# Optimization experiments

Measured on AMD Instinct MI355X. Metric: run time of the kernel, lower is better.

## Reference

```python
import jax, jax.numpy as jnp
import numpy as np

N_NODES = 50000
N_EDGES = 1000000
NODE_IN = 64
EDGE_OUT = 64
NODE_OUT = 64
GLOBAL_DIM = 64
N_GRAPHS = 64


def _glorot(key, shape):
    fan_in = shape[0]
    return (jax.random.normal(key, shape, dtype=jnp.float32) / jnp.sqrt(jnp.float32(fan_in)))


def setup_inputs() -> dict:
    key = jax.random.key(0)
    ks = jax.random.split(key, 12)
    x = jax.random.normal(ks[0], (N_NODES, NODE_IN), dtype=jnp.float32)
    edge_index = jax.random.randint(ks[1], (2, N_EDGES), 0, N_NODES, dtype=jnp.int64 if jax.config.jax_enable_x64 else jnp.int32)
    edge_attr = jax.random.normal(ks[2], (N_EDGES, EDGE_OUT), dtype=jnp.float32)
    u = jax.random.normal(ks[3], (N_GRAPHS, GLOBAL_DIM), dtype=jnp.float32)
    batch = jnp.sort(jax.random.randint(ks[4], (N_NODES,), 0, N_GRAPHS, dtype=jnp.int64 if jax.config.jax_enable_x64 else jnp.int32))
    # node_mlp_1: Linear(node_in+edge_out -> node_out), ReLU, Linear(node_out -> node_out)
    W1 = _glorot(ks[5], (NODE_IN + EDGE_OUT, NODE_OUT))
    b1 = jnp.zeros((NODE_OUT,), dtype=jnp.float32)
    W2 = _glorot(ks[6], (NODE_OUT, NODE_OUT))
    b2 = jnp.zeros((NODE_OUT,), dtype=jnp.float32)
    # node_mlp_2: Linear(global_dim+node_in+node_out -> node_out), ReLU, Linear(node_out -> node_out)
    W3 = _glorot(ks[7], (GLOBAL_DIM + NODE_IN + NODE_OUT, NODE_OUT))
    b3 = jnp.zeros((NODE_OUT,), dtype=jnp.float32)
    W4 = _glorot(ks[8], (NODE_OUT, NODE_OUT))
    b4 = jnp.zeros((NODE_OUT,), dtype=jnp.float32)
    return {"x": x, "edge_index": edge_index, "edge_attr": edge_attr, "u": u, "batch": batch,
            "W1": W1, "b1": b1, "W2": W2, "b2": b2, "W3": W3, "b3": b3, "W4": W4, "b4": b4}


def reference(x, edge_index, edge_attr, u, batch, W1, b1, W2, b2, W3, b3, W4, b4):
    row, col = edge_index[0], edge_index[1]
    # per-edge MLP on [x[row] || edge_attr]  -> [E, node_out]
    e = jnp.concatenate([x[row], edge_attr], axis=1)
    e = jnp.maximum(e @ W1 + b1, 0.0) @ W2 + b2
    # scatter_mean over destination nodes (zero where a node has no incoming edges)
    sums = jax.ops.segment_sum(e, col, num_segments=N_NODES)
    counts = jax.ops.segment_sum(jnp.ones((e.shape[0],), dtype=e.dtype), col, num_segments=N_NODES)
    agg = sums / jnp.clip(counts, 1.0)[:, None]
    # per-node MLP on [x || agg || u[batch]]
    h = jnp.concatenate([x, agg, u[batch]], axis=1)
    return jnp.maximum(h @ W3 + b3, 0.0) @ W4 + b4
```

## Files before the change

### kernel.cpp

```cpp
#include <hip/hip_runtime.h>

#define E_TOTAL 1000000
#define NN 50000
#define NB_SCAN ((NN + 255) / 256)

typedef __attribute__((ext_vector_type(8))) short bf16x8;
typedef __attribute__((ext_vector_type(8))) __bf16 bfv8;
typedef __attribute__((ext_vector_type(4))) float f32x4;
typedef __attribute__((ext_vector_type(4))) unsigned short u16x4;
typedef __attribute__((ext_vector_type(8))) unsigned short u16x8;

__device__ __forceinline__ float bf2f(unsigned short u) {
  unsigned int x = ((unsigned int)u) << 16;
  return __builtin_bit_cast(float, x);
}

__device__ __forceinline__ unsigned short f2bf(float v) {
  __bf16 b = (__bf16)v;
  return __builtin_bit_cast(unsigned short, b);
}

__device__ __forceinline__ bf16x8 pack8(float4 u, float4 v) {
  bfv8 f;
  f[0] = (__bf16)u.x; f[1] = (__bf16)u.y; f[2] = (__bf16)u.z; f[3] = (__bf16)u.w;
  f[4] = (__bf16)v.x; f[5] = (__bf16)v.y; f[6] = (__bf16)v.z; f[7] = (__bf16)v.w;
  return __builtin_bit_cast(bf16x8, f);
}

__device__ __forceinline__ bf16x8 cvt8(const float* __restrict__ p) {
  return pack8(*reinterpret_cast<const float4*>(p), *reinterpret_cast<const float4*>(p + 4));
}

__global__ void conv_kernel(const float* __restrict__ x, unsigned short* __restrict__ xb) {
  const int i = blockIdx.x * 256 + threadIdx.x;
  if (i < NN * 8) {
    const float4 v0 = *reinterpret_cast<const float4*>(x + (size_t)i * 8);
    const float4 v1 = *reinterpret_cast<const float4*>(x + (size_t)i * 8 + 4);
    bf16x8 p = pack8(v0, v1);
    *reinterpret_cast<bf16x8*>(xb + (size_t)i * 8) = p;
  }
}

__global__ void w3p_kernel(const float* __restrict__ W2, const float* __restrict__ W3,
                           const float* __restrict__ b2, float* __restrict__ W3p,
                           float* __restrict__ bb) {
  const int idx = blockIdx.x * 256 + threadIdx.x;
  if (idx < 64 * 64) {
    const int i = idx >> 6, j = idx & 63;
    float s = 0.f;
#pragma unroll 8
    for (int k = 0; k < 64; ++k) s += W2[i * 64 + k] * W3[(64 + k) * 64 + j];
    W3p[(64 + i) * 64 + j] = s;
    W3p[i * 64 + j] = W3[i * 64 + j];
    W3p[(128 + i) * 64 + j] = W3[(128 + i) * 64 + j];
  } else if (idx < 64 * 64 + 64) {
    const int j = idx - 64 * 64;
    float s = 0.f;
#pragma unroll 8
    for (int k = 0; k < 64; ++k) s += b2[k] * W3[(64 + k) * 64 + j];
    bb[j] = s;
  }
}


__global__ void hist_kernel(const int* __restrict__ ei, int* __restrict__ cnt) {
  int i = blockIdx.x * blockDim.x + threadIdx.x;
  if (i < E_TOTAL) atomicAdd(cnt + ei[E_TOTAL + i], 1);
}

__global__ void scan_block_kernel(const int* __restrict__ cnt, int* __restrict__ offs,
                                  int* __restrict__ btot) {
  __shared__ int s[256];
  const int tid = threadIdx.x;
  const int i = blockIdx.x * 256 + tid;
  int v = (i < NN) ? cnt[i] : 0;
  s[tid] = v;
  __syncthreads();
#pragma unroll
  for (int d = 1; d < 256; d <<= 1) {
    int t = (tid >= d) ? s[tid - d] : 0;
    __syncthreads();
    s[tid] += t;
    __syncthreads();
  }
  int incl = s[tid];
  if (i < NN) offs[i] = incl - v;
  if (tid == 255) btot[blockIdx.x] = incl;
}

__global__ void scan_add_kernel(int* __restrict__ offs, const int* __restrict__ btot,
                                int* __restrict__ run) {
  __shared__ int s[256];
  const int tid = threadIdx.x, bid = blockIdx.x;
  s[tid] = (tid < bid && tid < NB_SCAN) ? btot[tid] : 0;
  __syncthreads();
#pragma unroll
  for (int d = 128; d > 0; d >>= 1) {
    if (tid < d) s[tid] += s[tid + d];
    __syncthreads();
  }
  const int base = s[0];
  const int i = bid * 256 + tid;
  if (i < NN) {
    int o = offs[i] + base;
    offs[i] = o;
    run[i] = o;
  }
  if (i == 0) offs[NN] = E_TOTAL;
}

__global__ __launch_bounds__(512) void edge_kernel(
    const unsigned short* __restrict__ xb, const int* __restrict__ ei,
    const float* __restrict__ ea, const float* __restrict__ W1,
    const float* __restrict__ b1, unsigned short* __restrict__ hbuf,
    int* __restrict__ run) {
  __shared__ unsigned short wlds[16 * 512];
  const int tid = threadIdx.x;
  const int w = tid >> 6, l = tid & 63;
  const int c = l & 15, g = l >> 4;

  for (int idx = tid; idx < 16 * 512; idx += 512) {
    const int e = idx & 7, ll = (idx >> 3) & 63, ft = idx >> 9;
    const int s = ft >> 2, t = ft & 3;
    wlds[idx] = f2bf(W1[(s * 32 + (ll >> 4) * 8 + e) * 64 + t * 16 + (ll & 15)]);
  }
  __syncthreads();

  const int ebase0 = blockIdx.x * 512 + w * 64;
  if (ebase0 >= E_TOTAL) return;

  const int idx_all = ei[ebase0 + l];
  const int col_all = ei[E_TOTAL + ebase0 + l];
  const int pos_all = atomicAdd(run + col_all, 1);

  float b1v[4];
#pragma unroll
  for (int t = 0; t < 4; ++t) b1v[t] = b1[t * 16 + c];

  int idxc = __shfl(idx_all, c);
  const unsigned short* xp0 = xb + (size_t)idxc * 64 + g * 8;
  bf16x8 xa0 = *reinterpret_cast<const bf16x8*>(xp0);
  bf16x8 xa1 = *reinterpret_cast<const bf16x8*>(xp0 + 32);
  const float* ap0 = ea + (long)(ebase0 + c) * 64 + g * 8;
  float4 ac0 = *reinterpret_cast<const float4*>(ap0);
  float4 ac1 = *reinterpret_cast<const float4*>(ap0 + 4);
  float4 ac2 = *reinterpret_cast<const float4*>(ap0 + 32);
  float4 ac3 = *reinterpret_cast<const float4*>(ap0 + 36);

#pragma unroll 1
  for (int it = 0; it < 4; ++it) {
    const int ebc = ebase0 + it * 16;
    const bool hasnext = (it < 3);

    float4 an0, an1, an2, an3;
    int idxn = 0;
    if (hasnext) {
      idxn = __shfl(idx_all, (it + 1) * 16 + c);
      const float* apn = ea + (long)(ebc + 16 + c) * 64 + g * 8;
      an0 = *reinterpret_cast<const float4*>(apn);
      an1 = *reinterpret_cast<const float4*>(apn + 4);
      an2 = *reinterpret_cast<const float4*>(apn + 32);
      an3 = *reinterpret_cast<const float4*>(apn + 36);
    }

    bf16x8 a2 = pack8(ac0, ac1);
    bf16x8 a3 = pack8(ac2, ac3);

    f32x4 acc[4];
#pragma unroll
    for (int t = 0; t < 4; ++t) acc[t] = (f32x4){0.f, 0.f, 0.f, 0.f};
#pragma unroll
    for (int t = 0; t < 4; ++t) {
      bf16x8 wf0 = *reinterpret_cast<const bf16x8*>(wlds + ((0 * 4 + t) * 64 + l) * 8);
      bf16x8 wf1 = *reinterpret_cast<const bf16x8*>(wlds + ((1 * 4 + t) * 64 + l) * 8);
      bf16x8 wf2 = *reinterpret_cast<const bf16x8*>(wlds + ((2 * 4 + t) * 64 + l) * 8);
      bf16x8 wf3 = *reinterpret_cast<const bf16x8*>(wlds + ((3 * 4 + t) * 64 + l) * 8);
      acc[t] = __builtin_amdgcn_mfma_f32_16x16x32_bf16(xa0, wf0, acc[t], 0, 0, 0);
      acc[t] = __builtin_amdgcn_mfma_f32_16x16x32_bf16(xa1, wf1, acc[t], 0, 0, 0);
      acc[t] = __builtin_amdgcn_mfma_f32_16x16x32_bf16(a2, wf2, acc[t], 0, 0, 0);
      acc[t] = __builtin_amdgcn_mfma_f32_16x16x32_bf16(a3, wf3, acc[t], 0, 0, 0);
    }

    bf16x8 xan0, xan1;
    if (hasnext) {
      const unsigned short* xpn = xb + (size_t)idxn * 64 + g * 8;
      xan0 = *reinterpret_cast<const bf16x8*>(xpn);
      xan1 = *reinterpret_cast<const bf16x8*>(xpn + 32);
    }

#pragma unroll
    for (int r = 0; r < 4; ++r) {
      const int pos = __shfl(pos_all, it * 16 + g * 4 + r);
      u16x4 vv;
#pragma unroll
      for (int t = 0; t < 4; ++t) vv[t] = f2bf(fmaxf(acc[t][r] + b1v[t], 0.f));
      *reinterpret_cast<u16x4*>(hbuf + (size_t)pos * 64 + c * 4) = vv;
    }

    if (hasnext) {
      xa0 = xan0; xa1 = xan1;
      ac0 = an0; ac1 = an1; ac2 = an2; ac3 = an3;
    }
  }
}

__global__ __launch_bounds__(256, 1) void reduce_kernel(
    const unsigned short* __restrict__ hbuf, const int* __restrict__ offs,
    float* __restrict__ out) {
  const int l = threadIdx.x & 63, w = threadIdx.x >> 6;
  const int n = blockIdx.x * 4 + w;
  if (n >= NN) return;
  const int start = offs[n], end = offs[n + 1];
  const int slot = l >> 3, p8 = (l & 7) * 8;
  float acc[8];
#pragma unroll
  for (int k = 0; k < 8; ++k) acc[k] = 0.f;
  for (int j0 = start; j0 < end; j0 += 8) {
    const int j = j0 + slot;
    if (j < end) {
      u16x8 v = *reinterpret_cast<const u16x8*>(hbuf + (size_t)j * 64 + p8);
#pragma unroll
      for (int k = 0; k < 8; ++k) acc[k] += bf2f(v[k]);
    }
  }
#pragma unroll
  for (int k = 0; k < 8; ++k) {
    float v = acc[k];
    v += __shfl_xor(v, 8);
    v += __shfl_xor(v, 16);
    v += __shfl_xor(v, 32);
    acc[k] = v;
  }
  if (l < 8) {
    const float inv = 1.0f / fmaxf((float)(end - start), 1.0f);
#pragma unroll
    for (int j = 0; j < 8; ++j) {
      const int p = l * 8 + j;
      const int ch = (p & 3) * 16 + (p >> 2);
      out[(size_t)n * 64 + ch] = acc[j] * inv;
    }
  }
}

__global__ __launch_bounds__(256, 1) void node_kernel(
    const unsigned short* __restrict__ xb, const int* __restrict__ batch,
    const float* __restrict__ u, const float* __restrict__ W3p,
    const float* __restrict__ b3, const float* __restrict__ W4,
    const float* __restrict__ b4, const float* __restrict__ bb,
    const int* __restrict__ offs, float* __restrict__ out) {
  __shared__ unsigned short h_lds[4][16 * 72];
  const int tid = threadIdx.x;
  const int w = tid >> 6, l = tid & 63;
  const int c = l & 15, g = l >> 4;

  bf16x8 w3f[6][4];
#pragma unroll
  for (int s = 0; s < 6; ++s)
#pragma unroll
    for (int t = 0; t < 4; ++t) {
      const float* wp = W3p + (s * 32 + g * 8) * 64 + t * 16 + c;
      bfv8 f;
#pragma unroll
      for (int e = 0; e < 8; ++e) f[e] = (__bf16)wp[e * 64];
      w3f[s][t] = __builtin_bit_cast(bf16x8, f);
    }
  bf16x8 w4f[2][4];
#pragma unroll
  for (int s = 0; s < 2; ++s)
#pragma unroll
    for (int t = 0; t < 4; ++t) {
      const float* wp = W4 + (s * 32 + g * 8) * 64 + t * 16 + c;
      bfv8 f;
#pragma unroll
      for (int e = 0; e < 8; ++e) f[e] = (__bf16)wp[e * 64];
      w4f[s][t] = __builtin_bit_cast(bf16x8, f);
    }
  float b3v[4], b4v[4], bbv[4];
#pragma unroll
  for (int t = 0; t < 4; ++t) {
    b3v[t] = b3[t * 16 + c];
    b4v[t] = b4[t * 16 + c];
    bbv[t] = bb[t * 16 + c];
  }

  unsigned short* hl = h_lds[w];
  const int nbase0 = blockIdx.x * 256 + w * 64;
#pragma unroll 1
  for (int it = 0; it < 4; ++it) {
    const int nb = nbase0 + it * 16;
    if (nb >= NN) break;
    const int my_n = nb + c;
    const float* sp = out + (long)my_n * 64 + g * 8;
    const float* up = u + (long)batch[my_n] * 64 + g * 8;
    const float flag = (offs[my_n + 1] > offs[my_n]) ? 1.f : 0.f;
    const unsigned short* xp = xb + (size_t)my_n * 64 + g * 8;
    bf16x8 a0 = *reinterpret_cast<const bf16x8*>(xp);
    bf16x8 a1 = *reinterpret_cast<const bf16x8*>(xp + 32);
    bf16x8 a2 = cvt8(sp);
    bf16x8 a3 = cvt8(sp + 32);
    bf16x8 a4 = cvt8(up);
    bf16x8 a5 = cvt8(up + 32);

    f32x4 acc[4];
#pragma unroll
    for (int t = 0; t < 4; ++t) acc[t] = (f32x4){0.f, 0.f, 0.f, 0.f};
#pragma unroll
    for (int t = 0; t < 4; ++t) {
      acc[t] = __builtin_amdgcn_mfma_f32_16x16x32_bf16(a0, w3f[0][t], acc[t], 0, 0, 0);
      acc[t] = __builtin_amdgcn_mfma_f32_16x16x32_bf16(a1, w3f[1][t], acc[t], 0, 0, 0);
      acc[t] = __builtin_amdgcn_mfma_f32_16x16x32_bf16(a2, w3f[2][t], acc[t], 0, 0, 0);
      acc[t] = __builtin_amdgcn_mfma_f32_16x16x32_bf16(a3, w3f[3][t], acc[t], 0, 0, 0);
      acc[t] = __builtin_amdgcn_mfma_f32_16x16x32_bf16(a4, w3f[4][t], acc[t], 0, 0, 0);
      acc[t] = __builtin_amdgcn_mfma_f32_16x16x32_bf16(a5, w3f[5][t], acc[t], 0, 0, 0);
    }
#pragma unroll
    for (int r = 0; r < 4; ++r) {
      const float fr = __shfl(flag, g * 4 + r);
#pragma unroll
      for (int t = 0; t < 4; ++t) acc[t][r] += fr * bbv[t];
    }
#pragma unroll
    for (int t = 0; t < 4; ++t)
#pragma unroll
      for (int r = 0; r < 4; ++r)
        hl[(g * 4 + r) * 72 + t * 16 + c] = f2bf(fmaxf(acc[t][r] + b3v[t], 0.f));
    __builtin_amdgcn_wave_barrier();
    bf16x8 h0 = *reinterpret_cast<const bf16x8*>(hl + c * 72 + g * 8);
    bf16x8 h1 = *reinterpret_cast<const bf16x8*>(hl + c * 72 + 32 + g * 8);
    f32x4 o[4];
#pragma unroll
    for (int t = 0; t < 4; ++t) o[t] = (f32x4){0.f, 0.f, 0.f, 0.f};
#pragma unroll
    for (int t = 0; t < 4; ++t) {
      o[t] = __builtin_amdgcn_mfma_f32_16x16x32_bf16(h0, w4f[0][t], o[t], 0, 0, 0);
      o[t] = __builtin_amdgcn_mfma_f32_16x16x32_bf16(h1, w4f[1][t], o[t], 0, 0, 0);
    }
    __builtin_amdgcn_wave_barrier();
#pragma unroll
    for (int r = 0; r < 4; ++r) {
      const int nrow = nb + g * 4 + r;
#pragma unroll
      for (int t = 0; t < 4; ++t)
        out[(long)nrow * 64 + t * 16 + c] = o[t][r] + b4v[t];
    }
  }
}

extern "C" void kernel_launch(void* const* d_in, const int* in_sizes, int n_in,
                              void* d_out, int out_size, void* d_ws, size_t ws_size,
                              hipStream_t stream) {
  const float* x = (const float*)d_in[0];
  const int* ei = (const int*)d_in[1];
  const float* ea = (const float*)d_in[2];
  const float* u = (const float*)d_in[3];
  const int* batch = (const int*)d_in[4];
  const float* W1 = (const float*)d_in[5];
  const float* b1 = (const float*)d_in[6];
  const float* W2 = (const float*)d_in[7];
  const float* b2 = (const float*)d_in[8];
  const float* W3 = (const float*)d_in[9];
  const float* b3 = (const float*)d_in[10];
  const float* W4 = (const float*)d_in[11];
  const float* b4 = (const float*)d_in[12];
  float* out = (float*)d_out;

  const size_t HB_OFF = 0;
  const size_t OFFS_OFF = 128000000;
  const size_t RUN_OFF = 128400000;
  const size_t BTOT_OFF = 128800000;
  const size_t W3P_OFF = 128804096;
  const size_t BB_OFF = 128853248;
  const size_t XB_OFF = 128900000;

  unsigned short* hbuf = (unsigned short*)((char*)d_ws + HB_OFF);
  int* offs = (int*)((char*)d_ws + OFFS_OFF);
  int* run = (int*)((char*)d_ws + RUN_OFF);
  int* btot = (int*)((char*)d_ws + BTOT_OFF);
  float* W3p = (float*)((char*)d_ws + W3P_OFF);
  float* bbv = (float*)((char*)d_ws + BB_OFF);
  unsigned short* xbp = (unsigned short*)((char*)d_ws + XB_OFF);

  const int egrid = (E_TOTAL + 255) / 256;
  const int egrid512 = (E_TOTAL + 511) / 512;
  const int ngrid = (NN + 255) / 256;

  hipMemsetAsync(run, 0, (size_t)NN * sizeof(int), stream);
  conv_kernel<<<(NN * 8 + 255) / 256, 256, 0, stream>>>(x, xbp);
  w3p_kernel<<<(64 * 64 + 64 + 255) / 256, 256, 0, stream>>>(W2, W3, b2, W3p, bbv);
  hist_kernel<<<egrid, 256, 0, stream>>>(ei, run);
  scan_block_kernel<<<NB_SCAN, 256, 0, stream>>>(run, offs, btot);
  scan_add_kernel<<<NB_SCAN, 256, 0, stream>>>(offs, btot, run);
  edge_kernel<<<egrid512, 512, 0, stream>>>(xbp, ei, ea, W1, b1, hbuf, run);
  reduce_kernel<<<(NN + 3) / 4, 256, 0, stream>>>(hbuf, offs, out);
  node_kernel<<<ngrid, 256, 0, stream>>>(xbp, batch, u, W3p, b3, W4, b4, bbv, offs, out);
}
```

Before: 236.5 us.

## Write edge hidden rows sequentially and gather via CSR order index in reduce

Adds a scatter kernel that builds a CSR permutation of edge ids. The edge kernel can then write its hidden rows in original edge order, which gives coalesced writes, instead of scattering them to CSR positions. The reduce kernel gathers rows through the order index, trading coalesced reads for random 128-byte row reads. Edge attribute loads also switch to nontemporal loads. This path is used only when the workspace is large enough.

```diff
diff --git a/kernel.cpp b/kernel.cpp
--- a/kernel.cpp
+++ b/kernel.cpp
@@ -20,23 +20,27 @@
   return __builtin_bit_cast(unsigned short, b);
 }
 
-__device__ __forceinline__ bf16x8 pack8(float4 u, float4 v) {
+__device__ __forceinline__ bf16x8 pack8v(f32x4 u, f32x4 v) {
   bfv8 f;
-  f[0] = (__bf16)u.x; f[1] = (__bf16)u.y; f[2] = (__bf16)u.z; f[3] = (__bf16)u.w;
-  f[4] = (__bf16)v.x; f[5] = (__bf16)v.y; f[6] = (__bf16)v.z; f[7] = (__bf16)v.w;
+  f[0] = (__bf16)u[0]; f[1] = (__bf16)u[1]; f[2] = (__bf16)u[2]; f[3] = (__bf16)u[3];
+  f[4] = (__bf16)v[0]; f[5] = (__bf16)v[1]; f[6] = (__bf16)v[2]; f[7] = (__bf16)v[3];
   return __builtin_bit_cast(bf16x8, f);
 }
 
+__device__ __forceinline__ f32x4 ldnt4(const float* __restrict__ p) {
+  return __builtin_nontemporal_load(reinterpret_cast<const f32x4*>(p));
+}
+
 __device__ __forceinline__ bf16x8 cvt8(const float* __restrict__ p) {
-  return pack8(*reinterpret_cast<const float4*>(p), *reinterpret_cast<const float4*>(p + 4));
+  return pack8v(*reinterpret_cast<const f32x4*>(p), *reinterpret_cast<const f32x4*>(p + 4));
 }
 
 __global__ void conv_kernel(const float* __restrict__ x, unsigned short* __restrict__ xb) {
   const int i = blockIdx.x * 256 + threadIdx.x;
   if (i < NN * 8) {
-    const float4 v0 = *reinterpret_cast<const float4*>(x + (size_t)i * 8);
-    const float4 v1 = *reinterpret_cast<const float4*>(x + (size_t)i * 8 + 4);
-    bf16x8 p = pack8(v0, v1);
+    const f32x4 v0 = *reinterpret_cast<const f32x4*>(x + (size_t)i * 8);
+    const f32x4 v1 = *reinterpret_cast<const f32x4*>(x + (size_t)i * 8 + 4);
+    bf16x8 p = pack8v(v0, v1);
     *reinterpret_cast<bf16x8*>(xb + (size_t)i * 8) = p;
   }
 }
@@ -109,6 +113,16 @@
   if (i == 0) offs[NN] = E_TOTAL;
 }
 
+__global__ void scatter_kernel(const int* __restrict__ ei, int* __restrict__ run,
+                               int* __restrict__ order) {
+  int i = blockIdx.x * blockDim.x + threadIdx.x;
+  if (i < E_TOTAL) {
+    const int pos = atomicAdd(run + ei[E_TOTAL + i], 1);
+    order[pos] = i;
+  }
+}
+
+template <int SEQ>
 __global__ __launch_bounds__(512) void edge_kernel(
     const unsigned short* __restrict__ xb, const int* __restrict__ ei,
     const float* __restrict__ ea, const float* __restrict__ W1,
@@ -130,8 +144,11 @@
   if (ebase0 >= E_TOTAL) return;
 
   const int idx_all = ei[ebase0 + l];
-  const int col_all = ei[E_TOTAL + ebase0 + l];
-  const int pos_all = atomicAdd(run + col_all, 1);
+  int pos_all = 0;
+  if (!SEQ) {
+    const int col_all = ei[E_TOTAL + ebase0 + l];
+    pos_all = atomicAdd(run + col_all, 1);
+  }
 
   float b1v[4];
 #pragma unroll
@@ -142,29 +159,29 @@
   bf16x8 xa0 = *reinterpret_cast<const bf16x8*>(xp0);
   bf16x8 xa1 = *reinterpret_cast<const bf16x8*>(xp0 + 32);
   const float* ap0 = ea + (long)(ebase0 + c) * 64 + g * 8;
-  float4 ac0 = *reinterpret_cast<const float4*>(ap0);
-  float4 ac1 = *reinterpret_cast<const float4*>(ap0 + 4);
-  float4 ac2 = *reinterpret_cast<const float4*>(ap0 + 32);
-  float4 ac3 = *reinterpret_cast<const float4*>(ap0 + 36);
+  f32x4 ac0 = ldnt4(ap0);
+  f32x4 ac1 = ldnt4(ap0 + 4);
+  f32x4 ac2 = ldnt4(ap0 + 32);
+  f32x4 ac3 = ldnt4(ap0 + 36);
 
 #pragma unroll 1
   for (int it = 0; it < 4; ++it) {
     const int ebc = ebase0 + it * 16;
     const bool hasnext = (it < 3);
 
-    float4 an0, an1, an2, an3;
+    f32x4 an0, an1, an2, an3;
     int idxn = 0;
     if (hasnext) {
       idxn = __shfl(idx_all, (it + 1) * 16 + c);
       const float* apn = ea + (long)(ebc + 16 + c) * 64 + g * 8;
-      an0 = *reinterpret_cast<const float4*>(apn);
-      an1 = *reinterpret_cast<const float4*>(apn + 4);
-      an2 = *reinterpret_cast<const float4*>(apn + 32);
-      an3 = *reinterpret_cast<const float4*>(apn + 36);
-    }
-
-    bf16x8 a2 = pack8(ac0, ac1);
-    bf16x8 a3 = pack8(ac2, ac3);
+      an0 = ldnt4(apn);
+      an1 = ldnt4(apn + 4);
+      an2 = ldnt4(apn + 32);
+      an3 = ldnt4(apn + 36);
+    }
+
+    bf16x8 a2 = pack8v(ac0, ac1);
+    bf16x8 a3 = pack8v(ac2, ac3);
 
     f32x4 acc[4];
 #pragma unroll
@@ -190,11 +207,13 @@
 
 #pragma unroll
     for (int r = 0; r < 4; ++r) {
-      const int pos = __shfl(pos_all, it * 16 + g * 4 + r);
       u16x4 vv;
 #pragma unroll
       for (int t = 0; t < 4; ++t) vv[t] = f2bf(fmaxf(acc[t][r] + b1v[t], 0.f));
-      *reinterpret_cast<u16x4*>(hbuf + (size_t)pos * 64 + c * 4) = vv;
+      size_t row;
+      if (SEQ) row = (size_t)(ebc + g * 4 + r);
+      else     row = (size_t)__shfl(pos_all, it * 16 + g * 4 + r);
+      *reinterpret_cast<u16x4*>(hbuf + row * 64 + c * 4) = vv;
     }
 
     if (hasnext) {
@@ -204,9 +223,10 @@
   }
 }
 
+template <int ORD>
 __global__ __launch_bounds__(256, 1) void reduce_kernel(
-    const unsigned short* __restrict__ hbuf, const int* __restrict__ offs,
-    float* __restrict__ out) {
+    const unsigned short* __restrict__ hbuf, const int* __restrict__ order,
+    const int* __restrict__ offs, float* __restrict__ out) {
   const int l = threadIdx.x & 63, w = threadIdx.x >> 6;
   const int n = blockIdx.x * 4 + w;
   if (n >= NN) return;
@@ -218,7 +238,8 @@
   for (int j0 = start; j0 < end; j0 += 8) {
     const int j = j0 + slot;
     if (j < end) {
-      u16x8 v = *reinterpret_cast<const u16x8*>(hbuf + (size_t)j * 64 + p8);
+      const size_t e = ORD ? (size_t)order[j] : (size_t)j;
+      u16x8 v = *reinterpret_cast<const u16x8*>(hbuf + e * 64 + p8);
 #pragma unroll
       for (int k = 0; k < 8; ++k) acc[k] += bf2f(v[k]);
     }
@@ -371,6 +392,8 @@
   const size_t W3P_OFF = 128804096;
   const size_t BB_OFF = 128853248;
   const size_t XB_OFF = 128900000;
+  const size_t ORD_OFF = 135300000;
+  const size_t NEED_SEQ = 139300000;
 
   unsigned short* hbuf = (unsigned short*)((char*)d_ws + HB_OFF);
   int* offs = (int*)((char*)d_ws + OFFS_OFF);
@@ -379,6 +402,8 @@
   float* W3p = (float*)((char*)d_ws + W3P_OFF);
   float* bbv = (float*)((char*)d_ws + BB_OFF);
   unsigned short* xbp = (unsigned short*)((char*)d_ws + XB_OFF);
+  int* order = (int*)((char*)d_ws + ORD_OFF);
+  const bool seq = (ws_size >= NEED_SEQ);
 
   const int egrid = (E_TOTAL + 255) / 256;
   const int egrid512 = (E_TOTAL + 511) / 512;
@@ -390,7 +415,13 @@
   hist_kernel<<<egrid, 256, 0, stream>>>(ei, run);
   scan_block_kernel<<<NB_SCAN, 256, 0, stream>>>(run, offs, btot);
   scan_add_kernel<<<NB_SCAN, 256, 0, stream>>>(offs, btot, run);
-  edge_kernel<<<egrid512, 512, 0, stream>>>(xbp, ei, ea, W1, b1, hbuf, run);
-  reduce_kernel<<<(NN + 3) / 4, 256, 0, stream>>>(hbuf, offs, out);
+  if (seq) {
+    scatter_kernel<<<egrid, 256, 0, stream>>>(ei, run, order);
+    edge_kernel<1><<<egrid512, 512, 0, stream>>>(xbp, ei, ea, W1, b1, hbuf, nullptr);
+    reduce_kernel<1><<<(NN + 3) / 4, 256, 0, stream>>>(hbuf, order, offs, out);
+  } else {
+    edge_kernel<0><<<egrid512, 512, 0, stream>>>(xbp, ei, ea, W1, b1, hbuf, run);
+    reduce_kernel<0><<<(NN + 3) / 4, 256, 0, stream>>>(hbuf, nullptr, offs, out);
+  }
   node_kernel<<<ngrid, 256, 0, stream>>>(xbp, batch, u, W3p, b3, W4, b4, bbv, offs, out);
 }
```

Result: slower. 282.2 us (+19.3%).

## Replace CSR sort-and-reduce with packed bf16 atomic scatter-add into node sums

Applied to the files above, without the earlier changes.

Drops the scan kernels, the per-edge position atomics, the 128MB per-edge hidden buffer and the segmented reduce kernel. Edges now scatter their ReLU hidden activations directly into a per-node bf16 sum buffer using global_atomic_pk_add_bf16, and the node kernel divides by the histogram count. The channel permutation is folded into the W2·W3 precompute. This removes a large write and read-back of per-edge data, but accumulates in bf16 through atomics, so precision drops with about 20 edges per node, and atomic contention may cost throughput.

```diff
diff --git a/kernel.cpp b/kernel.cpp
--- a/kernel.cpp
+++ b/kernel.cpp
@@ -2,12 +2,10 @@
 
 #define E_TOTAL 1000000
 #define NN 50000
-#define NB_SCAN ((NN + 255) / 256)
 
 typedef __attribute__((ext_vector_type(8))) short bf16x8;
 typedef __attribute__((ext_vector_type(8))) __bf16 bfv8;
 typedef __attribute__((ext_vector_type(4))) float f32x4;
-typedef __attribute__((ext_vector_type(4))) unsigned short u16x4;
 typedef __attribute__((ext_vector_type(8))) unsigned short u16x8;
 
 __device__ __forceinline__ float bf2f(unsigned short u) {
@@ -20,23 +18,27 @@
   return __builtin_bit_cast(unsigned short, b);
 }
 
-__device__ __forceinline__ bf16x8 pack8(float4 u, float4 v) {
+__device__ __forceinline__ bf16x8 pack8v(f32x4 u, f32x4 v) {
   bfv8 f;
-  f[0] = (__bf16)u.x; f[1] = (__bf16)u.y; f[2] = (__bf16)u.z; f[3] = (__bf16)u.w;
-  f[4] = (__bf16)v.x; f[5] = (__bf16)v.y; f[6] = (__bf16)v.z; f[7] = (__bf16)v.w;
+  f[0] = (__bf16)u[0]; f[1] = (__bf16)u[1]; f[2] = (__bf16)u[2]; f[3] = (__bf16)u[3];
+  f[4] = (__bf16)v[0]; f[5] = (__bf16)v[1]; f[6] = (__bf16)v[2]; f[7] = (__bf16)v[3];
   return __builtin_bit_cast(bf16x8, f);
 }
 
 __device__ __forceinline__ bf16x8 cvt8(const float* __restrict__ p) {
-  return pack8(*reinterpret_cast<const float4*>(p), *reinterpret_cast<const float4*>(p + 4));
+  return pack8v(*reinterpret_cast<const f32x4*>(p), *reinterpret_cast<const f32x4*>(p + 4));
+}
+
+__device__ __forceinline__ void pk_atomic_add_bf16(unsigned short* addr, unsigned int packed) {
+  asm volatile("global_atomic_pk_add_bf16 %0, %1, off" :: "v"(addr), "v"(packed));
 }
 
 __global__ void conv_kernel(const float* __restrict__ x, unsigned short* __restrict__ xb) {
   const int i = blockIdx.x * 256 + threadIdx.x;
   if (i < NN * 8) {
-    const float4 v0 = *reinterpret_cast<const float4*>(x + (size_t)i * 8);
-    const float4 v1 = *reinterpret_cast<const float4*>(x + (size_t)i * 8 + 4);
-    bf16x8 p = pack8(v0, v1);
+    const f32x4 v0 = *reinterpret_cast<const f32x4*>(x + (size_t)i * 8);
+    const f32x4 v1 = *reinterpret_cast<const f32x4*>(x + (size_t)i * 8 + 4);
+    bf16x8 p = pack8v(v0, v1);
     *reinterpret_cast<bf16x8*>(xb + (size_t)i * 8) = p;
   }
 }
@@ -46,13 +48,14 @@
                            float* __restrict__ bb) {
   const int idx = blockIdx.x * 256 + threadIdx.x;
   if (idx < 64 * 64) {
-    const int i = idx >> 6, j = idx & 63;
+    const int p = idx >> 6, j = idx & 63;
+    const int chp = (p & 3) * 16 + (p >> 2);
     float s = 0.f;
 #pragma unroll 8
-    for (int k = 0; k < 64; ++k) s += W2[i * 64 + k] * W3[(64 + k) * 64 + j];
-    W3p[(64 + i) * 64 + j] = s;
-    W3p[i * 64 + j] = W3[i * 64 + j];
-    W3p[(128 + i) * 64 + j] = W3[(128 + i) * 64 + j];
+    for (int k = 0; k < 64; ++k) s += W2[chp * 64 + k] * W3[(64 + k) * 64 + j];
+    W3p[(64 + p) * 64 + j] = s;
+    W3p[p * 64 + j] = W3[p * 64 + j];
+    W3p[(128 + p) * 64 + j] = W3[(128 + p) * 64 + j];
   } else if (idx < 64 * 64 + 64) {
     const int j = idx - 64 * 64;
     float s = 0.f;
@@ -62,58 +65,15 @@
   }
 }
 
-
 __global__ void hist_kernel(const int* __restrict__ ei, int* __restrict__ cnt) {
   int i = blockIdx.x * blockDim.x + threadIdx.x;
   if (i < E_TOTAL) atomicAdd(cnt + ei[E_TOTAL + i], 1);
 }
 
-__global__ void scan_block_kernel(const int* __restrict__ cnt, int* __restrict__ offs,
-                                  int* __restrict__ btot) {
-  __shared__ int s[256];
-  const int tid = threadIdx.x;
-  const int i = blockIdx.x * 256 + tid;
-  int v = (i < NN) ? cnt[i] : 0;
-  s[tid] = v;
-  __syncthreads();
-#pragma unroll
-  for (int d = 1; d < 256; d <<= 1) {
-    int t = (tid >= d) ? s[tid - d] : 0;
-    __syncthreads();
-    s[tid] += t;
-    __syncthreads();
-  }
-  int incl = s[tid];
-  if (i < NN) offs[i] = incl - v;
-  if (tid == 255) btot[blockIdx.x] = incl;
-}
-
-__global__ void scan_add_kernel(int* __restrict__ offs, const int* __restrict__ btot,
-                                int* __restrict__ run) {
-  __shared__ int s[256];
-  const int tid = threadIdx.x, bid = blockIdx.x;
-  s[tid] = (tid < bid && tid < NB_SCAN) ? btot[tid] : 0;
-  __syncthreads();
-#pragma unroll
-  for (int d = 128; d > 0; d >>= 1) {
-    if (tid < d) s[tid] += s[tid + d];
-    __syncthreads();
-  }
-  const int base = s[0];
-  const int i = bid * 256 + tid;
-  if (i < NN) {
-    int o = offs[i] + base;
-    offs[i] = o;
-    run[i] = o;
-  }
-  if (i == 0) offs[NN] = E_TOTAL;
-}
-
 __global__ __launch_bounds__(512) void edge_kernel(
     const unsigned short* __restrict__ xb, const int* __restrict__ ei,
     const float* __restrict__ ea, const float* __restrict__ W1,
-    const float* __restrict__ b1, unsigned short* __restrict__ hbuf,
-    int* __restrict__ run) {
+    const float* __restrict__ b1, unsigned short* __restrict__ sums) {
   __shared__ unsigned short wlds[16 * 512];
   const int tid = threadIdx.x;
   const int w = tid >> 6, l = tid & 63;
@@ -131,7 +91,6 @@
 
   const int idx_all = ei[ebase0 + l];
   const int col_all = ei[E_TOTAL + ebase0 + l];
-  const int pos_all = atomicAdd(run + col_all, 1);
 
   float b1v[4];
 #pragma unroll
@@ -142,29 +101,29 @@
   bf16x8 xa0 = *reinterpret_cast<const bf16x8*>(xp0);
   bf16x8 xa1 = *reinterpret_cast<const bf16x8*>(xp0 + 32);
   const float* ap0 = ea + (long)(ebase0 + c) * 64 + g * 8;
-  float4 ac0 = *reinterpret_cast<const float4*>(ap0);
-  float4 ac1 = *reinterpret_cast<const float4*>(ap0 + 4);
-  float4 ac2 = *reinterpret_cast<const float4*>(ap0 + 32);
-  float4 ac3 = *reinterpret_cast<const float4*>(ap0 + 36);
+  f32x4 ac0 = *reinterpret_cast<const f32x4*>(ap0);
+  f32x4 ac1 = *reinterpret_cast<const f32x4*>(ap0 + 4);
+  f32x4 ac2 = *reinterpret_cast<const f32x4*>(ap0 + 32);
+  f32x4 ac3 = *reinterpret_cast<const f32x4*>(ap0 + 36);
 
 #pragma unroll 1
   for (int it = 0; it < 4; ++it) {
+    const bool hasnext = (it < 3);
     const int ebc = ebase0 + it * 16;
-    const bool hasnext = (it < 3);
-
-    float4 an0, an1, an2, an3;
+
+    f32x4 an0, an1, an2, an3;
     int idxn = 0;
     if (hasnext) {
       idxn = __shfl(idx_all, (it + 1) * 16 + c);
       const float* apn = ea + (long)(ebc + 16 + c) * 64 + g * 8;
-      an0 = *reinterpret_cast<const float4*>(apn);
-      an1 = *reinterpret_cast<const float4*>(apn + 4);
-      an2 = *reinterpret_cast<const float4*>(apn + 32);
-      an3 = *reinterpret_cast<const float4*>(apn + 36);
-    }
-
-    bf16x8 a2 = pack8(ac0, ac1);
-    bf16x8 a3 = pack8(ac2, ac3);
+      an0 = *reinterpret_cast<const f32x4*>(apn);
+      an1 = *reinterpret_cast<const f32x4*>(apn + 4);
+      an2 = *reinterpret_cast<const f32x4*>(apn + 32);
+      an3 = *reinterpret_cast<const f32x4*>(apn + 36);
+    }
+
+    bf16x8 a2 = pack8v(ac0, ac1);
+    bf16x8 a3 = pack8v(ac2, ac3);
 
     f32x4 acc[4];
 #pragma unroll
@@ -190,54 +149,19 @@
 
 #pragma unroll
     for (int r = 0; r < 4; ++r) {
-      const int pos = __shfl(pos_all, it * 16 + g * 4 + r);
-      u16x4 vv;
-#pragma unroll
-      for (int t = 0; t < 4; ++t) vv[t] = f2bf(fmaxf(acc[t][r] + b1v[t], 0.f));
-      *reinterpret_cast<u16x4*>(hbuf + (size_t)pos * 64 + c * 4) = vv;
+      const int node = __shfl(col_all, it * 16 + g * 4 + r);
+      unsigned short v0 = f2bf(fmaxf(acc[0][r] + b1v[0], 0.f));
+      unsigned short v1 = f2bf(fmaxf(acc[1][r] + b1v[1], 0.f));
+      unsigned short v2 = f2bf(fmaxf(acc[2][r] + b1v[2], 0.f));
+      unsigned short v3 = f2bf(fmaxf(acc[3][r] + b1v[3], 0.f));
+      unsigned short* base = sums + (size_t)node * 64 + c * 4;
+      pk_atomic_add_bf16(base, (unsigned int)v0 | ((unsigned int)v1 << 16));
+      pk_atomic_add_bf16(base + 2, (unsigned int)v2 | ((unsigned int)v3 << 16));
     }
 
     if (hasnext) {
       xa0 = xan0; xa1 = xan1;
       ac0 = an0; ac1 = an1; ac2 = an2; ac3 = an3;
-    }
-  }
-}
-
-__global__ __launch_bounds__(256, 1) void reduce_kernel(
-    const unsigned short* __restrict__ hbuf, const int* __restrict__ offs,
-    float* __restrict__ out) {
-  const int l = threadIdx.x & 63, w = threadIdx.x >> 6;
-  const int n = blockIdx.x * 4 + w;
-  if (n >= NN) return;
-  const int start = offs[n], end = offs[n + 1];
-  const int slot = l >> 3, p8 = (l & 7) * 8;
-  float acc[8];
-#pragma unroll
-  for (int k = 0; k < 8; ++k) acc[k] = 0.f;
-  for (int j0 = start; j0 < end; j0 += 8) {
-    const int j = j0 + slot;
-    if (j < end) {
-      u16x8 v = *reinterpret_cast<const u16x8*>(hbuf + (size_t)j * 64 + p8);
-#pragma unroll
-      for (int k = 0; k < 8; ++k) acc[k] += bf2f(v[k]);
-    }
-  }
-#pragma unroll
-  for (int k = 0; k < 8; ++k) {
-    float v = acc[k];
-    v += __shfl_xor(v, 8);
-    v += __shfl_xor(v, 16);
-    v += __shfl_xor(v, 32);
-    acc[k] = v;
-  }
-  if (l < 8) {
-    const float inv = 1.0f / fmaxf((float)(end - start), 1.0f);
-#pragma unroll
-    for (int j = 0; j < 8; ++j) {
-      const int p = l * 8 + j;
-      const int ch = (p & 3) * 16 + (p >> 2);
-      out[(size_t)n * 64 + ch] = acc[j] * inv;
     }
   }
 }
@@ -247,7 +171,8 @@
     const float* __restrict__ u, const float* __restrict__ W3p,
     const float* __restrict__ b3, const float* __restrict__ W4,
     const float* __restrict__ b4, const float* __restrict__ bb,
-    const int* __restrict__ offs, float* __restrict__ out) {
+    const int* __restrict__ cnt, const unsigned short* __restrict__ sums,
+    float* __restrict__ out) {
   __shared__ unsigned short h_lds[4][16 * 72];
   const int tid = threadIdx.x;
   const int w = tid >> 6, l = tid & 63;
@@ -290,14 +215,24 @@
     const int nb = nbase0 + it * 16;
     if (nb >= NN) break;
     const int my_n = nb + c;
-    const float* sp = out + (long)my_n * 64 + g * 8;
+    const int cn = cnt[my_n];
+    const float inv = 1.0f / fmaxf((float)cn, 1.0f);
+    const float flag = (cn > 0) ? 1.f : 0.f;
     const float* up = u + (long)batch[my_n] * 64 + g * 8;
-    const float flag = (offs[my_n + 1] > offs[my_n]) ? 1.f : 0.f;
     const unsigned short* xp = xb + (size_t)my_n * 64 + g * 8;
     bf16x8 a0 = *reinterpret_cast<const bf16x8*>(xp);
     bf16x8 a1 = *reinterpret_cast<const bf16x8*>(xp + 32);
-    bf16x8 a2 = cvt8(sp);
-    bf16x8 a3 = cvt8(sp + 32);
+    const unsigned short* sp = sums + (size_t)my_n * 64 + g * 8;
+    u16x8 s0 = *reinterpret_cast<const u16x8*>(sp);
+    u16x8 s1 = *reinterpret_cast<const u16x8*>(sp + 32);
+    bfv8 f2, f3;
+#pragma unroll
+    for (int e = 0; e < 8; ++e) {
+      f2[e] = (__bf16)(bf2f(s0[e]) * inv);
+      f3[e] = (__bf16)(bf2f(s1[e]) * inv);
+    }
+    bf16x8 a2 = __builtin_bit_cast(bf16x8, f2);
+    bf16x8 a3 = __builtin_bit_cast(bf16x8, f3);
     bf16x8 a4 = cvt8(up);
     bf16x8 a5 = cvt8(up + 32);
 
@@ -364,33 +299,27 @@
   const float* b4 = (const float*)d_in[12];
   float* out = (float*)d_out;
 
-  const size_t HB_OFF = 0;
-  const size_t OFFS_OFF = 128000000;
-  const size_t RUN_OFF = 128400000;
-  const size_t BTOT_OFF = 128800000;
-  const size_t W3P_OFF = 128804096;
-  const size_t BB_OFF = 128853248;
-  const size_t XB_OFF = 128900000;
-
-  unsigned short* hbuf = (unsigned short*)((char*)d_ws + HB_OFF);
-  int* offs = (int*)((char*)d_ws + OFFS_OFF);
-  int* run = (int*)((char*)d_ws + RUN_OFF);
-  int* btot = (int*)((char*)d_ws + BTOT_OFF);
+  const size_t SUM_OFF = 0;
+  const size_t CNT_OFF = 6400000;
+  const size_t XB_OFF = 6600064;
+  const size_t W3P_OFF = 13000064;
+  const size_t BB_OFF = 13049216;
+
+  unsigned short* sums = (unsigned short*)((char*)d_ws + SUM_OFF);
+  int* cnt = (int*)((char*)d_ws + CNT_OFF);
+  unsigned short* xbp = (unsigned short*)((char*)d_ws + XB_OFF);
   float* W3p = (float*)((char*)d_ws + W3P_OFF);
   float* bbv = (float*)((char*)d_ws + BB_OFF);
-  unsigned short* xbp = (unsigned short*)((char*)d_ws + XB_OFF);
 
   const int egrid = (E_TOTAL + 255) / 256;
   const int egrid512 = (E_TOTAL + 511) / 512;
   const int ngrid = (NN + 255) / 256;
 
-  hipMemsetAsync(run, 0, (size_t)NN * sizeof(int), stream);
+  hipMemsetAsync(sums, 0, (size_t)NN * 64 * sizeof(unsigned short), stream);
+  hipMemsetAsync(cnt, 0, (size_t)NN * sizeof(int), stream);
   conv_kernel<<<(NN * 8 + 255) / 256, 256, 0, stream>>>(x, xbp);
   w3p_kernel<<<(64 * 64 + 64 + 255) / 256, 256, 0, stream>>>(W2, W3, b2, W3p, bbv);
-  hist_kernel<<<egrid, 256, 0, stream>>>(ei, run);
-  scan_block_kernel<<<NB_SCAN, 256, 0, stream>>>(run, offs, btot);
-  scan_add_kernel<<<NB_SCAN, 256, 0, stream>>>(offs, btot, run);
-  edge_kernel<<<egrid512, 512, 0, stream>>>(xbp, ei, ea, W1, b1, hbuf, run);
-  reduce_kernel<<<(NN + 3) / 4, 256, 0, stream>>>(hbuf, offs, out);
-  node_kernel<<<ngrid, 256, 0, stream>>>(xbp, batch, u, W3p, b3, W4, b4, bbv, offs, out);
-}
+  hist_kernel<<<egrid, 256, 0, stream>>>(ei, cnt);
+  edge_kernel<<<egrid512, 512, 0, stream>>>(xbp, ei, ea, W1, b1, sums);
+  node_kernel<<<ngrid, 256, 0, stream>>>(xbp, batch, u, W3p, b3, W4, b4, bbv, cnt, sums, out);
+}
```

Result: slower. 291.9 us (+23.4%).
